# Kernel optimization log

Hardware: AMD Instinct MI355X
Metric: run time of the kernel (lower is better)

The kernel has to match this reference:

```python
import jax, jax.numpy as jnp
import numpy as np

N_NODES = 400
HID = 96
DEC = 64
FEAT_STATIC = 8
FEAT = FEAT_STATIC + N_NODES  # 408
EPS = 1e-8


def prelu(x, a):
    # single-parameter PReLU (torch default num_parameters=1)
    return jnp.where(x >= 0, x, a * x)


def setup_inputs() -> dict:
    key = jax.random.key(0)
    ks = jax.random.split(key, 16)
    B = 16
    E = N_NODES * (N_NODES - 1) // 2  # 79800

    x = jax.random.normal(ks[0], (B, E), dtype=jnp.float32)
    node_features = jax.random.normal(ks[1], (B, N_NODES, FEAT_STATIC), dtype=jnp.float32)
    sc_matrix = jax.random.uniform(ks[2], (B, N_NODES, N_NODES), dtype=jnp.float32)

    # normalization buffers (computed from train split in torch; random stand-ins)
    static_mean = jax.random.normal(ks[3], (1, 1, FEAT_STATIC), dtype=jnp.float32) * 0.1
    static_std = jnp.ones((1, 1, FEAT_STATIC), dtype=jnp.float32)

    def lin(k, fin, fout):
        kw, kb = jax.random.split(k)
        lim = 1.0 / np.sqrt(fin)
        W = jax.random.uniform(kw, (fin, fout), minval=-lim, maxval=lim, dtype=jnp.float32)
        b = jax.random.uniform(kb, (fout,), minval=-lim, maxval=lim, dtype=jnp.float32)
        return W, b

    W_e1, b_e1 = lin(ks[4], FEAT, HID)
    W_e2, b_e2 = lin(ks[5], HID, HID)
    W_d1, b_d1 = lin(ks[6], 3 * HID, DEC)  # symmetric decoder: 3 * node_embed_dim
    W_d2, b_d2 = lin(ks[7], DEC, DEC)
    W_d3, b_d3 = lin(ks[8], DEC, 1)

    a25 = jnp.float32(0.25)

    ei_np, ej_np = np.triu_indices(N_NODES, k=1)
    ei = jnp.asarray(ei_np, dtype=jnp.int32)
    ej = jnp.asarray(ej_np, dtype=jnp.int32)

    return {
        "x": x, "node_features": node_features, "sc_matrix": sc_matrix,
        "static_mean": static_mean, "static_std": static_std,
        "W_e1": W_e1, "b_e1": b_e1, "a_e1": a25,
        "W_e2": W_e2, "b_e2": b_e2, "a_e2": a25,
        "W_d1": W_d1, "b_d1": b_d1, "a_d1": a25,
        "W_d2": W_d2, "b_d2": b_d2, "a_d2": a25,
        "W_d3": W_d3, "b_d3": b_d3,
        "ei": ei, "ej": ej,
    }


def reference(x, node_features, sc_matrix, static_mean, static_std,
              W_e1, b_e1, a_e1, W_e2, b_e2, a_e2,
              W_d1, b_d1, a_d1, W_d2, b_d2, a_d2, W_d3, b_d3, ei, ej):
    # x (SC upper triangle) is only used for batch size in the torch module.
    # static anatomical block: z-score with train stats
    s = (node_features - static_mean) / (static_std + EPS)  # [B,N,8]
    # sc_row block, 'brain_scale': divide by per-matrix mean
    m = sc_matrix / jnp.maximum(
        jnp.mean(sc_matrix, axis=(-2, -1), keepdims=True), EPS)  # [B,N,N]
    feats = jnp.concatenate([s, m], axis=-1)  # [B,N,408]

    # shared node encoder (dropout inactive at eval)
    h = prelu(feats @ W_e1 + b_e1, a_e1)
    h = prelu(h @ W_e2 + b_e2, a_e2)  # [B,N,96]

    # per-edge gather over upper-triangle indices
    h_i = h[:, ei, :]  # [B,E,96]
    h_j = h[:, ej, :]
    # symmetric edge features
    edge_feat = jnp.concatenate(
        [h_i + h_j, jnp.abs(h_i - h_j), h_i * h_j], axis=-1)  # [B,E,288]

    z = prelu(edge_feat @ W_d1 + b_d1, a_d1)
    z = prelu(z @ W_d2 + b_d2, a_d2)
    out = (z @ W_d3 + b_d3)[..., 0]  # [B,E]
    return out
```

## Files before the change

kernel.cpp:

```cpp
#include <hip/hip_runtime.h>

#define NN 400
#define HID 96
#define EDGES 79800
#define BATCH 16
#define ROWS (BATCH*EDGES)
#define NT 13
#define NPAIRS 91

typedef _Float16 f16;
typedef f16 f16x2 __attribute__((ext_vector_type(2)));
typedef f16 f16x8 __attribute__((ext_vector_type(8)));
typedef __fp16 fp16x2 __attribute__((ext_vector_type(2)));
typedef float f32x16 __attribute__((ext_vector_type(16)));
typedef unsigned int u32;
typedef unsigned long long u64;

union H8 { f16x8 h; u32 u[4]; f16x2 p[4]; fp16x2 q[4]; u64 d[2]; };
union C2 { f16x2 h; fp16x2 q; u32 u; };

__device__ inline f16x2 pkrtz(float a, float b) {
  C2 c; c.q = __builtin_amdgcn_cvt_pkrtz(a, b); return c.h;
}
__device__ inline u32 pkrtz_u(float a, float b) {
  C2 c; c.q = __builtin_amdgcn_cvt_pkrtz(a, b); return c.u;
}
__device__ inline float fdot2a(f16x2 a, f16x2 b, float c) {
#if __has_builtin(__builtin_amdgcn_fdot2)
  C2 ca, cb; ca.h = a; cb.h = b;
  return __builtin_amdgcn_fdot2(ca.q, cb.q, c, false);
#else
  return c + (float)a.x*(float)b.x + (float)a.y*(float)b.y;
#endif
}

__device__ inline f16x8 habs8(f16x8 x) {
  H8 t; t.h = x;
  t.u[0] &= 0x7fff7fffu; t.u[1] &= 0x7fff7fffu;
  t.u[2] &= 0x7fff7fffu; t.u[3] &= 0x7fff7fffu;
  return t.h;
}

__device__ inline f16x8 pack8(float a0,float a1,float a2,float a3,
                              float a4,float a5,float a6,float a7){
  H8 u;
  u.p[0] = pkrtz(a0,a1);
  u.p[1] = pkrtz(a2,a3);
  u.p[2] = pkrtz(a4,a5);
  u.p[3] = pkrtz(a6,a7);
  return u.h;
}

__device__ inline void plswap(u32 &x, u32 &y) {
  auto r = __builtin_amdgcn_permlane32_swap((int)x, (int)y, false, false);
  x = (u32)r[0]; y = (u32)r[1];
}

#define MEMFENCE asm volatile("" ::: "memory")

__global__ void prep_mean_kernel(const float* __restrict__ We1, const float* __restrict__ We2,
                                 const float* __restrict__ W1, const float* __restrict__ W2,
                                 const float* __restrict__ sc,
                                 u32* __restrict__ wq, float* __restrict__ mpart) {
  if (blockIdx.x >= 140) {
    int p = blockIdx.x - 140;
    int b = p >> 4, part = p & 15;
    const float4* src = (const float4*)(sc + (size_t)b*160000) + part*2500;
    float s = 0.f;
    for (int i = threadIdx.x; i < 2500; i += 256) {
      float4 v = src[i];
      s += (v.x + v.y) + (v.z + v.w);
    }
    __shared__ float red[256];
    red[threadIdx.x] = s; __syncthreads();
    for (int off = 128; off > 0; off >>= 1) {
      if (threadIdx.x < off) red[threadIdx.x] += red[threadIdx.x + off];
      __syncthreads();
    }
    if (threadIdx.x == 0) mpart[p] = red[0];
    return;
  }
  int D = blockIdx.x*256 + threadIdx.x;
  float v0, v1;
  if (D < 9216) {
    int frag = D >> 8;  int t = frag >> 1, q = frag & 1;
    int rem = D & 255;  int lane = rem >> 2, dj = rem & 3;
    int c = lane & 31, h2 = lane >> 5;
    int k = 16*t + 8*h2 + 2*dj;
    int d = 32*q + c;
    v0 = W1[k*64 + d]; v1 = W1[(k+1)*64 + d];
  } else if (D < 11264) {
    int Dl = D - 9216;
    int frag = Dl >> 8; int t2 = frag >> 1, q = frag & 1;
    int rem = Dl & 255; int lane = rem >> 2, dj = rem & 3;
    int c = lane & 31, h2 = lane >> 5;
    int k = 16*t2 + 8*h2 + 2*dj;
    int d = 32*q + c;
    v0 = W2[k*64 + d]; v1 = W2[(k+1)*64 + d];
  } else if (D < 31232) {
    int Dl = D - 11264;
    int frag = Dl >> 8; int t = frag/3, ct = frag - 3*t;
    int rem = Dl & 255; int lane = rem >> 2, dj = rem & 3;
    int c = lane & 31, h2 = lane >> 5;
    int k0 = 16*t + 8*h2 + 2*dj, k1 = k0 + 1;
    int d = 32*ct + c;
    v0 = (k0 < 400) ? We1[(8+k0)*96 + d] : (k0 < 408 ? We1[(k0-400)*96 + d] : 0.f);
    v1 = (k1 < 400) ? We1[(8+k1)*96 + d] : (k1 < 408 ? We1[(k1-400)*96 + d] : 0.f);
  } else {
    int Dl = D - 31232;
    int frag = Dl >> 8; int t = frag/3, ct = frag - 3*t;
    int rem = Dl & 255; int lane = rem >> 2, dj = rem & 3;
    int c = lane & 31, h2 = lane >> 5;
    int k = 16*t + 8*h2 + 2*dj;
    int d = 32*ct + c;
    v0 = We2[k*96 + d]; v1 = We2[(k+1)*96 + d];
  }
  wq[D] = pkrtz_u(v0, v1);
}

__global__ __launch_bounds__(256) void enc_kernel(
    const float* __restrict__ sc, const float* __restrict__ nf,
    const float* __restrict__ smean, const float* __restrict__ sstd,
    const float* __restrict__ be1, const float* __restrict__ ae1,
    const float* __restrict__ be2, const float* __restrict__ ae2,
    const float* __restrict__ mpart, const u32* __restrict__ wq,
    f16* __restrict__ hout) {
  __shared__ u32 lds[6720 + 1600];
  const int tid = threadIdx.x;
  const int wid = tid >> 6, lane = tid & 63;
  const int c = lane & 31, h2 = lane >> 5;
  const int r0 = blockIdx.x * 32;
  {
    int row = tid >> 3, seg = tid & 7;
    int r = r0 + row;
    int b = r / 400;
    float ms = 0.f;
    const float4* mp4 = (const float4*)(mpart + 16*b);
#pragma unroll
    for (int k = 0; k < 4; ++k) { float4 v = mp4[k]; ms += (v.x+v.y)+(v.z+v.w); }
    float rm = 1.f / fmaxf(ms*(1.f/160000.f), 1e-8f);
    const float4* src = (const float4*)(sc + (size_t)r*400);
#pragma unroll
    for (int i = 0; i < 13; ++i) {
      int col4 = seg + 8*i;
      if (col4 < 100) {
        float4 v = src[col4];
        u32 lo = pkrtz_u(v.x*rm, v.y*rm);
        u32 hi = pkrtz_u(v.z*rm, v.w*rm);
        *(u64*)(lds + row*210 + col4*2) = (u64)lo | ((u64)hi << 32);
      }
    }
  }
  f16x8 bfr[26], we2r[6], af25;
  if (wid < 3) {
    const u32* wb1 = wq + 11264;
#pragma unroll
    for (int t = 0; t < 26; ++t)
      bfr[t] = *(const f16x8*)(wb1 + ((t*3+wid)*64 + lane)*4);
    const u32* wb2 = wq + 31232;
#pragma unroll
    for (int t = 0; t < 6; ++t)
      we2r[t] = *(const f16x8*)(wb2 + ((t*3+wid)*64 + lane)*4);
    af25 = (f16x8){};
    if (h2 == 0) {
      int r = r0 + c;
      float q0[8];
#pragma unroll
      for (int j = 0; j < 8; ++j)
        q0[j] = (nf[r*8 + j] - smean[j]) / (sstd[j] + 1e-8f);
      af25 = pack8(q0[0],q0[1],q0[2],q0[3],q0[4],q0[5],q0[6],q0[7]);
    }
  }
  __syncthreads();
  f16* zb16 = (f16*)(lds + 6720);
  if (wid < 3) {
    const float a1 = *ae1;
    float bv = be1[32*wid + c];
    f32x16 acc;
#pragma unroll
    for (int i = 0; i < 16; ++i) acc[i] = bv;
#pragma unroll
    for (int t = 0; t < 25; ++t) {
      H8 av;
      const u32* ap = lds + c*210 + 8*t + 4*h2;
      av.d[0] = *(const u64*)ap;
      av.d[1] = *(const u64*)(ap + 2);
      acc = __builtin_amdgcn_mfma_f32_32x32x16_f16(av.h, bfr[t], acc, 0,0,0);
    }
    acc = __builtin_amdgcn_mfma_f32_32x32x16_f16(af25, bfr[25], acc, 0,0,0);
#pragma unroll
    for (int r = 0; r < 16; ++r) {
      float v = acc[r]; v = fmaxf(v, a1*v);
      int row = (r & 3) + 8*(r >> 2) + 4*h2;
      zb16[row*100 + 32*wid + c] = (f16)v;
    }
  }
  __syncthreads();
  if (wid < 3) {
    const float a2 = *ae2;
    float bv = be2[32*wid + c];
    f32x16 acc2;
#pragma unroll
    for (int i = 0; i < 16; ++i) acc2[i] = bv;
#pragma unroll
    for (int t = 0; t < 6; ++t) {
      f16x8 af = *(const f16x8*)(zb16 + c*100 + 16*t + 8*h2);
      acc2 = __builtin_amdgcn_mfma_f32_32x32x16_f16(af, we2r[t], acc2, 0,0,0);
    }
#pragma unroll
    for (int rr = 0; rr < 16; ++rr) {
      int row = (rr & 3) + 8*(rr >> 2) + 4*h2;
      float v = acc2[rr]; v = fmaxf(v, a2*v);
      hout[(r0 + row)*96 + 32*wid + c] = (f16)v;
    }
  }
}

__global__ __launch_bounds__(256, 3) void decoder_kernel(
    const f16* __restrict__ hbuf, const u32* __restrict__ wq,
    const float* __restrict__ b1, const float* __restrict__ b2,
    const float* __restrict__ ad1, const float* __restrict__ ad2,
    const float* __restrict__ W3, const float* __restrict__ b3p,
    float* __restrict__ out) {
  __shared__ alignas(16) u32 smem[12800];
  const int tid = threadIdx.x;
  int p = blockIdx.x;
  int b = p / NPAIRS, pr = p - b*NPAIRS;
  int I = 0;
  while (pr >= NT - I) { pr -= NT - I; ++I; }
  const int J = I + pr;
  for (int i = tid; i < 384; i += 256) {
    int row = i / 12, off = i - row*12;
    int nb = I*32 + row; nb = nb < NN ? nb : NN-1;
    const float4* src = (const float4*)(hbuf + (size_t)(b*NN + nb)*HID) + off;
    *((float4*)(smem + row*48) + off) = *src;
  }
  {
    float4* dst = (float4*)(smem + 1536);
    const float4* srcw = (const float4*)wq;
    for (int i = tid; i < 2816; i += 256) dst[i] = srcw[i];
  }

  const int lane = tid & 63;
  const int wid  = tid >> 6;
  const int c = lane & 31, h2 = lane >> 5;
  const int gj = J*32 + c;
  const int gjc = gj < NN ? gj : NN-1;
  f16x8 hjr[6];
  {
    const f16* hjp = hbuf + (size_t)(b*NN + gjc)*HID + 8*h2;
#pragma unroll
    for (int t = 0; t < 6; ++t) hjr[t] = *(const f16x8*)(hjp + 16*t);
  }
  const float a1 = *ad1, a2 = *ad2, b3 = *b3p;
  const f16x2 a1v = pkrtz(a1, a1);
  const f16x2 a2v = pkrtz(a2, a2);
  f16x8 bcst = (f16x8){};
  f16x8 ab1f[2]; ab1f[0] = (f16x8){}; ab1f[1] = (f16x8){};
  f16x8 ab2f[2]; ab2f[0] = (f16x8){}; ab2f[1] = (f16x8){};
  if (h2 == 0) {
    bcst[0] = (f16)1.f;
    ab1f[0][0] = (f16)b1[c];      ab1f[1][0] = (f16)b1[32 + c];
    ab2f[0][0] = (f16)b2[c];      ab2f[1][0] = (f16)b2[32 + c];
  }
  f16x2 w3q[2][8];
#pragma unroll
  for (int q2 = 0; q2 < 2; ++q2)
#pragma unroll
    for (int a = 0; a < 8; ++a) {
      int base = 32*q2 + 8*(a >> 1) + 2*(a & 1) + 4*h2;
      w3q[q2][a] = pkrtz(W3[base], W3[base + 1]);
    }
  __syncthreads();

  const f16* hIb = (const f16*)smem;
  const u32* wfr = smem + 1536;
  const u32* w2a = smem + 10752;
  const int bofs = b*EDGES;

#pragma unroll 1
  for (int it = 0; it < 4; ++it) {
#pragma unroll 1
    for (int m = 0; m < 2; ++m) {
      MEMFENCE;
      const int irow = it*8 + wid*2 + m;
      const f16* hip_ = hIb + irow*HID;
      f32x16 acc[2] = {};
      acc[0] = __builtin_amdgcn_mfma_f32_32x32x16_f16(ab1f[0], bcst, acc[0], 0,0,0);
      acc[1] = __builtin_amdgcn_mfma_f32_32x32x16_f16(ab1f[1], bcst, acc[1], 0,0,0);
#pragma unroll
      for (int t = 0; t < 6; ++t) {
        MEMFENCE;
        f16x8 as0 = *(const f16x8*)(wfr + (((t    )*2+0)*64 + lane)*4);
        f16x8 as1 = *(const f16x8*)(wfr + (((t    )*2+1)*64 + lane)*4);
        f16x8 ad0 = *(const f16x8*)(wfr + (((t+ 6)*2+0)*64 + lane)*4);
        f16x8 ad1_ = *(const f16x8*)(wfr + (((t+ 6)*2+1)*64 + lane)*4);
        f16x8 ap0 = *(const f16x8*)(wfr + (((t+12)*2+0)*64 + lane)*4);
        f16x8 ap1 = *(const f16x8*)(wfr + (((t+12)*2+1)*64 + lane)*4);
        f16x8 hj8 = hjr[t];
        f16x8 hi8 = *(const f16x8*)(hip_ + 16*t + 8*h2);
        f16x8 su = hi8 + hj8;
        f16x8 di = habs8(hi8 - hj8);
        f16x8 prd = hi8 * hj8;
        __builtin_amdgcn_s_setprio(1);
        acc[0] = __builtin_amdgcn_mfma_f32_32x32x16_f16(as0, su,  acc[0], 0,0,0);
        acc[1] = __builtin_amdgcn_mfma_f32_32x32x16_f16(as1, su,  acc[1], 0,0,0);
        acc[0] = __builtin_amdgcn_mfma_f32_32x32x16_f16(ad0, di,  acc[0], 0,0,0);
        acc[1] = __builtin_amdgcn_mfma_f32_32x32x16_f16(ad1_, di, acc[1], 0,0,0);
        acc[0] = __builtin_amdgcn_mfma_f32_32x32x16_f16(ap0, prd, acc[0], 0,0,0);
        acc[1] = __builtin_amdgcn_mfma_f32_32x32x16_f16(ap1, prd, acc[1], 0,0,0);
        __builtin_amdgcn_s_setprio(0);
      }
      u32 w[16];
#pragma unroll
      for (int q = 0; q < 2; ++q)
#pragma unroll
        for (int a = 0; a < 8; ++a) {
          f16x2 pz = pkrtz(acc[q][2*a], acc[q][2*a+1]);
          pz = __builtin_elementwise_max(pz, pz * a1v);
          C2 cv; cv.h = pz; w[q*8 + a] = cv.u;
        }
#pragma unroll
      for (int g = 0; g < 4; ++g) {
        plswap(w[g*4+0], w[g*4+2]);
        plswap(w[g*4+1], w[g*4+3]);
      }
      f32x16 zacc[2] = {};
      zacc[0] = __builtin_amdgcn_mfma_f32_32x32x16_f16(ab2f[0], bcst, zacc[0], 0,0,0);
      zacc[1] = __builtin_amdgcn_mfma_f32_32x32x16_f16(ab2f[1], bcst, zacc[1], 0,0,0);
#pragma unroll
      for (int t2 = 0; t2 < 4; ++t2) {
        MEMFENCE;
        H8 zf; zf.u[0] = w[4*t2]; zf.u[1] = w[4*t2+1]; zf.u[2] = w[4*t2+2]; zf.u[3] = w[4*t2+3];
        f16x8 w20 = *(const f16x8*)(w2a + ((t2*2+0)*64 + lane)*4);
        f16x8 w21 = *(const f16x8*)(w2a + ((t2*2+1)*64 + lane)*4);
        __builtin_amdgcn_s_setprio(1);
        zacc[0] = __builtin_amdgcn_mfma_f32_32x32x16_f16(w20, zf.h, zacc[0], 0,0,0);
        zacc[1] = __builtin_amdgcn_mfma_f32_32x32x16_f16(w21, zf.h, zacc[1], 0,0,0);
        __builtin_amdgcn_s_setprio(0);
      }
      float s0 = 0.f, s1 = 0.f;
#pragma unroll
      for (int a = 0; a < 8; ++a) {
        f16x2 pz0 = pkrtz(zacc[0][2*a], zacc[0][2*a+1]);
        pz0 = __builtin_elementwise_max(pz0, pz0 * a2v);
        s0 = fdot2a(pz0, w3q[0][a], s0);
        f16x2 pz1 = pkrtz(zacc[1][2*a], zacc[1][2*a+1]);
        pz1 = __builtin_elementwise_max(pz1, pz1 * a2v);
        s1 = fdot2a(pz1, w3q[1][a], s1);
      }
      float ssum = s0 + s1;
      ssum += __shfl_xor(ssum, 32);
      int gi = I*32 + irow;
      if (h2 == 0 && gi < gj && gj < NN) {
        int eo = bofs + gi*(799 - gi)/2 + (gj - gi - 1);
        out[eo] = ssum + b3;
      }
    }
  }
}

extern "C" void kernel_launch(void* const* d_in, const int* in_sizes, int n_in,
                              void* d_out, int out_size, void* d_ws, size_t ws_size,
                              hipStream_t stream) {
  const float* nf  = (const float*)d_in[1];
  const float* sc  = (const float*)d_in[2];
  const float* sm  = (const float*)d_in[3];
  const float* ss  = (const float*)d_in[4];
  const float* We1 = (const float*)d_in[5];
  const float* be1 = (const float*)d_in[6];
  const float* ae1 = (const float*)d_in[7];
  const float* We2 = (const float*)d_in[8];
  const float* be2 = (const float*)d_in[9];
  const float* ae2 = (const float*)d_in[10];
  const float* W1  = (const float*)d_in[11];
  const float* b1  = (const float*)d_in[12];
  const float* a1  = (const float*)d_in[13];
  const float* W2  = (const float*)d_in[14];
  const float* b2  = (const float*)d_in[15];
  const float* a2  = (const float*)d_in[16];
  const float* W3  = (const float*)d_in[17];
  const float* b3  = (const float*)d_in[18];
  float* out = (float*)d_out;

  char* ws = (char*)d_ws;
  float* mpart = (float*)ws;
  f16*   hbuf = (f16*)(ws + 1024);
  u32*   wq   = (u32*)(ws + 1024 + 1228800);

  prep_mean_kernel<<<396, 256, 0, stream>>>(We1, We2, W1, W2, sc, wq, mpart);
  enc_kernel<<<200, 256, 0, stream>>>(sc, nf, sm, ss, be1, ae1, be2, ae2,
                                      mpart, wq, hbuf);
  decoder_kernel<<<BATCH*NPAIRS, 256, 0, stream>>>(hbuf, wq, b1, b2, a1, a2,
                                                   W3, b3, out);
}
```

Baseline: 183.8 us.

## Share decoder weight fragments across two rows and move biases/W3 to LDS

Interchanges the decoder loops so that each wave computes two i-rows at once, loading each first-layer weight fragment from LDS once and applying it to both rows. Biases are now read from LDS straight into the accumulators instead of being injected through an extra MFMA with a ones vector. The W3 fragments move from registers to LDS reads. The aim is to halve the LDS weight traffic per row, drop the bias MFMAs and free registers, at the cost of holding twice the accumulator state (64 floats for acc) at the same launch bounds, which may raise register pressure.

```diff
diff --git a/kernel.cpp b/kernel.cpp
--- a/kernel.cpp
+++ b/kernel.cpp
@@ -222,7 +222,7 @@
     const float* __restrict__ ad1, const float* __restrict__ ad2,
     const float* __restrict__ W3, const float* __restrict__ b3p,
     float* __restrict__ out) {
-  __shared__ alignas(16) u32 smem[12800];
+  __shared__ alignas(16) u32 smem[12960];
   const int tid = threadIdx.x;
   int p = blockIdx.x;
   int b = p / NPAIRS, pr = p - b*NPAIRS;
@@ -240,6 +240,15 @@
     const float4* srcw = (const float4*)wq;
     for (int i = tid; i < 2816; i += 256) dst[i] = srcw[i];
   }
+  if (tid < 64) {
+    ((float*)(smem + 12800))[tid] = b1[tid];
+    ((float*)(smem + 12864))[tid] = b2[tid];
+  }
+  if (tid < 32) {
+    int hh = tid >> 4, rem = tid & 15, q2 = rem >> 3, a = rem & 7;
+    int base = 32*q2 + 8*(a >> 1) + 2*(a & 1) + 4*hh;
+    smem[12928 + tid] = pkrtz_u(W3[base], W3[base + 1]);
+  }
 
   const int lane = tid & 63;
   const int wid  = tid >> 6;
@@ -255,68 +264,67 @@
   const float a1 = *ad1, a2 = *ad2, b3 = *b3p;
   const f16x2 a1v = pkrtz(a1, a1);
   const f16x2 a2v = pkrtz(a2, a2);
-  f16x8 bcst = (f16x8){};
-  f16x8 ab1f[2]; ab1f[0] = (f16x8){}; ab1f[1] = (f16x8){};
-  f16x8 ab2f[2]; ab2f[0] = (f16x8){}; ab2f[1] = (f16x8){};
-  if (h2 == 0) {
-    bcst[0] = (f16)1.f;
-    ab1f[0][0] = (f16)b1[c];      ab1f[1][0] = (f16)b1[32 + c];
-    ab2f[0][0] = (f16)b2[c];      ab2f[1][0] = (f16)b2[32 + c];
-  }
-  f16x2 w3q[2][8];
-#pragma unroll
-  for (int q2 = 0; q2 < 2; ++q2)
-#pragma unroll
-    for (int a = 0; a < 8; ++a) {
-      int base = 32*q2 + 8*(a >> 1) + 2*(a & 1) + 4*h2;
-      w3q[q2][a] = pkrtz(W3[base], W3[base + 1]);
-    }
   __syncthreads();
 
   const f16* hIb = (const f16*)smem;
   const u32* wfr = smem + 1536;
   const u32* w2a = smem + 10752;
+  const float* b1f = (const float*)(smem + 12800);
+  const float* b2f = (const float*)(smem + 12864);
+  const u32* w3l = smem + 12928;
   const int bofs = b*EDGES;
 
 #pragma unroll 1
   for (int it = 0; it < 4; ++it) {
-#pragma unroll 1
-    for (int m = 0; m < 2; ++m) {
+    MEMFENCE;
+    const int i0 = it*8 + wid*2;
+    const f16* hi0 = hIb + (i0+0)*HID;
+    const f16* hi1 = hIb + (i0+1)*HID;
+    f32x16 acc[2][2];
+#pragma unroll
+    for (int q = 0; q < 2; ++q)
+#pragma unroll
+      for (int a = 0; a < 8; ++a) {
+        int base = 32*q + 8*(a >> 1) + 2*(a & 1) + 4*h2;
+        float2 bv = *(const float2*)(b1f + base);
+        acc[0][q][2*a] = bv.x; acc[0][q][2*a+1] = bv.y;
+        acc[1][q][2*a] = bv.x; acc[1][q][2*a+1] = bv.y;
+      }
+#pragma unroll
+    for (int t = 0; t < 6; ++t) {
       MEMFENCE;
-      const int irow = it*8 + wid*2 + m;
-      const f16* hip_ = hIb + irow*HID;
-      f32x16 acc[2] = {};
-      acc[0] = __builtin_amdgcn_mfma_f32_32x32x16_f16(ab1f[0], bcst, acc[0], 0,0,0);
-      acc[1] = __builtin_amdgcn_mfma_f32_32x32x16_f16(ab1f[1], bcst, acc[1], 0,0,0);
-#pragma unroll
-      for (int t = 0; t < 6; ++t) {
-        MEMFENCE;
-        f16x8 as0 = *(const f16x8*)(wfr + (((t    )*2+0)*64 + lane)*4);
-        f16x8 as1 = *(const f16x8*)(wfr + (((t    )*2+1)*64 + lane)*4);
-        f16x8 ad0 = *(const f16x8*)(wfr + (((t+ 6)*2+0)*64 + lane)*4);
-        f16x8 ad1_ = *(const f16x8*)(wfr + (((t+ 6)*2+1)*64 + lane)*4);
-        f16x8 ap0 = *(const f16x8*)(wfr + (((t+12)*2+0)*64 + lane)*4);
-        f16x8 ap1 = *(const f16x8*)(wfr + (((t+12)*2+1)*64 + lane)*4);
-        f16x8 hj8 = hjr[t];
-        f16x8 hi8 = *(const f16x8*)(hip_ + 16*t + 8*h2);
+      f16x8 as0 = *(const f16x8*)(wfr + (((t    )*2+0)*64 + lane)*4);
+      f16x8 as1 = *(const f16x8*)(wfr + (((t    )*2+1)*64 + lane)*4);
+      f16x8 ad0 = *(const f16x8*)(wfr + (((t+ 6)*2+0)*64 + lane)*4);
+      f16x8 ad1_ = *(const f16x8*)(wfr + (((t+ 6)*2+1)*64 + lane)*4);
+      f16x8 ap0 = *(const f16x8*)(wfr + (((t+12)*2+0)*64 + lane)*4);
+      f16x8 ap1 = *(const f16x8*)(wfr + (((t+12)*2+1)*64 + lane)*4);
+      f16x8 hj8 = hjr[t];
+#pragma unroll
+      for (int m = 0; m < 2; ++m) {
+        f16x8 hi8 = *(const f16x8*)((m ? hi1 : hi0) + 16*t + 8*h2);
         f16x8 su = hi8 + hj8;
         f16x8 di = habs8(hi8 - hj8);
         f16x8 prd = hi8 * hj8;
         __builtin_amdgcn_s_setprio(1);
-        acc[0] = __builtin_amdgcn_mfma_f32_32x32x16_f16(as0, su,  acc[0], 0,0,0);
-        acc[1] = __builtin_amdgcn_mfma_f32_32x32x16_f16(as1, su,  acc[1], 0,0,0);
-        acc[0] = __builtin_amdgcn_mfma_f32_32x32x16_f16(ad0, di,  acc[0], 0,0,0);
-        acc[1] = __builtin_amdgcn_mfma_f32_32x32x16_f16(ad1_, di, acc[1], 0,0,0);
-        acc[0] = __builtin_amdgcn_mfma_f32_32x32x16_f16(ap0, prd, acc[0], 0,0,0);
-        acc[1] = __builtin_amdgcn_mfma_f32_32x32x16_f16(ap1, prd, acc[1], 0,0,0);
+        acc[m][0] = __builtin_amdgcn_mfma_f32_32x32x16_f16(as0, su,  acc[m][0], 0,0,0);
+        acc[m][1] = __builtin_amdgcn_mfma_f32_32x32x16_f16(as1, su,  acc[m][1], 0,0,0);
+        acc[m][0] = __builtin_amdgcn_mfma_f32_32x32x16_f16(ad0, di,  acc[m][0], 0,0,0);
+        acc[m][1] = __builtin_amdgcn_mfma_f32_32x32x16_f16(ad1_, di, acc[m][1], 0,0,0);
+        acc[m][0] = __builtin_amdgcn_mfma_f32_32x32x16_f16(ap0, prd, acc[m][0], 0,0,0);
+        acc[m][1] = __builtin_amdgcn_mfma_f32_32x32x16_f16(ap1, prd, acc[m][1], 0,0,0);
         __builtin_amdgcn_s_setprio(0);
       }
+    }
+#pragma unroll
+    for (int m = 0; m < 2; ++m) {
+      MEMFENCE;
       u32 w[16];
 #pragma unroll
       for (int q = 0; q < 2; ++q)
 #pragma unroll
         for (int a = 0; a < 8; ++a) {
-          f16x2 pz = pkrtz(acc[q][2*a], acc[q][2*a+1]);
+          f16x2 pz = pkrtz(acc[m][q][2*a], acc[m][q][2*a+1]);
           pz = __builtin_elementwise_max(pz, pz * a1v);
           C2 cv; cv.h = pz; w[q*8 + a] = cv.u;
         }
@@ -325,9 +333,15 @@
         plswap(w[g*4+0], w[g*4+2]);
         plswap(w[g*4+1], w[g*4+3]);
       }
-      f32x16 zacc[2] = {};
-      zacc[0] = __builtin_amdgcn_mfma_f32_32x32x16_f16(ab2f[0], bcst, zacc[0], 0,0,0);
-      zacc[1] = __builtin_amdgcn_mfma_f32_32x32x16_f16(ab2f[1], bcst, zacc[1], 0,0,0);
+      f32x16 zacc[2];
+#pragma unroll
+      for (int q = 0; q < 2; ++q)
+#pragma unroll
+        for (int a = 0; a < 8; ++a) {
+          int base = 32*q + 8*(a >> 1) + 2*(a & 1) + 4*h2;
+          float2 bv = *(const float2*)(b2f + base);
+          zacc[q][2*a] = bv.x; zacc[q][2*a+1] = bv.y;
+        }
 #pragma unroll
       for (int t2 = 0; t2 < 4; ++t2) {
         MEMFENCE;
@@ -342,16 +356,18 @@
       float s0 = 0.f, s1 = 0.f;
 #pragma unroll
       for (int a = 0; a < 8; ++a) {
+        C2 wv0; wv0.u = w3l[(h2 << 4) | a];
         f16x2 pz0 = pkrtz(zacc[0][2*a], zacc[0][2*a+1]);
         pz0 = __builtin_elementwise_max(pz0, pz0 * a2v);
-        s0 = fdot2a(pz0, w3q[0][a], s0);
+        s0 = fdot2a(pz0, wv0.h, s0);
+        C2 wv1; wv1.u = w3l[(h2 << 4) | 8 | a];
         f16x2 pz1 = pkrtz(zacc[1][2*a], zacc[1][2*a+1]);
         pz1 = __builtin_elementwise_max(pz1, pz1 * a2v);
-        s1 = fdot2a(pz1, w3q[1][a], s1);
+        s1 = fdot2a(pz1, wv1.h, s1);
       }
       float ssum = s0 + s1;
       ssum += __shfl_xor(ssum, 32);
-      int gi = I*32 + irow;
+      int gi = I*32 + i0 + m;
       if (h2 == 0 && gi < gj && gj < NN) {
         int eo = bofs + gi*(799 - gi)/2 + (gj - gi - 1);
         out[eo] = ssum + b3;
```

New measurement: 178.6 us. 2.8% less time.
